# Performance work log

Measured on AMD Instinct MI355X. Metric: run time of the kernel, lower is better.

Reference implementation:

```python
import jax, jax.numpy as jnp
import numpy as np

B, H, V, MSG_MAX_LEN = 16384, 512, 32, 20


def setup_inputs() -> dict:
    key = jax.random.key(0)
    ks = jax.random.split(key, 8)
    s = 0.05  # weight scale so softmax stays well-conditioned
    return {
        "encoder_hidden": jax.random.normal(ks[0], (B, H), jnp.float32),
        "encoder_cell": jax.random.normal(ks[1], (B, H), jnp.float32),
        "W_ih": jax.random.normal(ks[2], (4 * H, V), jnp.float32) * s,
        "b_ih": jax.random.normal(ks[3], (4 * H,), jnp.float32) * s,
        "W_hh": jax.random.normal(ks[4], (4 * H, H), jnp.float32) * s,
        "b_hh": jax.random.normal(ks[5], (4 * H,), jnp.float32) * s,
        "W_out": jax.random.normal(ks[6], (V, H), jnp.float32) * s,
        "b_out": jax.random.normal(ks[7], (V,), jnp.float32) * s,
        "init_input": jnp.zeros((1, V), jnp.float32),
        "eos_idx": 31,
    }


def reference(encoder_hidden, encoder_cell, W_ih, b_ih, W_hh, b_hh, W_out, b_out, init_input, eos_idx):
    batch = encoder_hidden.shape[0]
    vocab = W_out.shape[0]
    # Original code never updates decoder_input (typo 'deocder_input'), so the
    # LSTM input is init_input every step -> input projection is loop-invariant.
    x = jnp.broadcast_to(init_input, (batch, init_input.shape[1]))
    x_proj = x @ W_ih.T + b_ih  # [B, 4H]

    def step(carry, _):
        h, c, mask, lp = carry  # h,c: [B,H]; mask: [1,B]; lp: scalar
        mask_out = mask  # mask is appended BEFORE the update in the original
        gates = x_proj + h @ W_hh.T + b_hh
        i, f, g, o = jnp.split(gates, 4, axis=1)  # torch LSTMCell gate order i,f,g,o
        i = jax.nn.sigmoid(i); f = jax.nn.sigmoid(f)
        g = jnp.tanh(g); o = jax.nn.sigmoid(o)
        c = f * c + i * g
        h = o * jnp.tanh(c)
        probs = jax.nn.softmax(h @ W_out.T + b_out, axis=1)  # [B,V]
        predict = jax.nn.one_hot(jnp.argmax(probs, axis=1), vocab, dtype=probs.dtype)  # eval-mode branch
        lp = lp + jnp.log((probs * predict).sum(axis=1)) @ mask[0]
        new_mask = mask * (1.0 - predict[:, eos_idx])  # zero out finished sequences
        return (h, c, new_mask, lp), (predict, mask_out)

    init = (encoder_hidden, encoder_cell,
            jnp.ones((1, batch), encoder_hidden.dtype),
            jnp.zeros((), encoder_hidden.dtype))
    (_, _, _, log_probs), (message, mask) = jax.lax.scan(step, init, None, length=MSG_MAX_LEN)
    return message, mask, log_probs  # [L,B,V], [L,1,B], scalar
```

## Files before the change

kernel.cpp:

```cpp
#include <hip/hip_runtime.h>
#include <math.h>

#define BATCH 16384
#define HDIM  512
#define VOCAB 32
#define STEPS 20
#define G4    2048

typedef _Float16 f16;
typedef _Float16 f16x8 __attribute__((ext_vector_type(8)));
typedef float    f32x16 __attribute__((ext_vector_type(16)));

#define SH   256.0f
#define SW   1024.0f
#define SINV (1.0f / (SH * SW))


__device__ __forceinline__ void gload16(const void* g, void* l) {
#if defined(__has_builtin) && __has_builtin(__builtin_amdgcn_global_load_lds)
    __builtin_amdgcn_global_load_lds(
        (const __attribute__((address_space(1))) void*)g,
        (__attribute__((address_space(3))) void*)l, 16, 0, 0);
#else
    *(float4*)l = *(const float4*)g;
#endif
}

__device__ __forceinline__ float fsig(float x)  { return 1.0f / (1.0f + __expf(-x)); }
__device__ __forceinline__ float ftanh(float x) { return 1.0f - 2.0f / (__expf(2.0f * x) + 1.0f); }

__global__ void init_xb_kernel(const float* __restrict__ W_ih,
                               const float* __restrict__ b_ih,
                               const float* __restrict__ b_hh,
                               const float* __restrict__ x0,
                               float* __restrict__ xb) {
    int n = blockIdx.x * blockDim.x + threadIdx.x;
    if (n >= G4) return;
    float s = b_ih[n] + b_hh[n];
    const float* wr = W_ih + (size_t)n * VOCAB;
    #pragma unroll
    for (int v = 0; v < VOCAB; v++) s += wr[v] * x0[v];
    xb[n] = s;
}

__global__ void init_mask_kernel(float* __restrict__ mask) {
    int b = blockIdx.x * blockDim.x + threadIdx.x;
    if (b < BATCH) mask[b] = 1.0f;
}

__global__ void wimg_kernel(const float* __restrict__ W_hh,
                            f16* __restrict__ Wh, f16* __restrict__ Wl) {
    size_t g  = (size_t)blockIdx.x * 256 + threadIdx.x;
    int ln = g & 63;  size_t r = g >> 6;
    int gg = r & 3;   size_t r2 = r >> 2;
    int ks = r2 & 1;  size_t r3 = r2 >> 1;
    int kc = r3 & 15; int jb = (int)(r3 >> 4);
    int n = gg * 512 + jb * 32 + (ln & 31);
    int k = kc * 32 + ks * 16 + (ln >> 5) * 8;
    const float* s = W_hh + (size_t)n * HDIM + k;
    f16x8 vh, vl;
    #pragma unroll
    for (int i = 0; i < 8; i++) {
        float x = s[i] * SW;
        f16 h = (f16)x;
        vh[i] = h;
        vl[i] = (f16)(x - (float)h);
    }
    *(f16x8*)(Wh + g * 8) = vh;
    *(f16x8*)(Wl + g * 8) = vl;
}

__global__ void woutimg_kernel(const float* __restrict__ W_out,
                               f16* __restrict__ Oh, f16* __restrict__ Ol) {
    int g  = blockIdx.x * 256 + threadIdx.x;
    int ln = g & 63;
    int r  = g >> 6;
    int kc = r >> 1, ks = r & 1;
    int v  = ln & 31;
    int k  = kc * 32 + ks * 16 + (ln >> 5) * 8;
    const float* s = W_out + (size_t)v * HDIM + k;
    f16x8 vh, vl;
    #pragma unroll
    for (int i = 0; i < 8; i++) {
        float x = s[i] * SW;
        f16 h = (f16)x;
        vh[i] = h;
        vl[i] = (f16)(x - (float)h);
    }
    *(f16x8*)(Oh + (size_t)g * 8) = vh;
    *(f16x8*)(Ol + (size_t)g * 8) = vl;
}

__global__ void hT_init_kernel(const float* __restrict__ src,
                               f16* __restrict__ dh, f16* __restrict__ dl) {
    size_t g = (size_t)blockIdx.x * 256 + threadIdx.x;
    int ln = g & 63;  size_t r = g >> 6;
    int mb = (int)(r & 511); int kk = (int)(r >> 9);
    int m = mb * 32 + (ln & 31);
    int k = kk * 16 + (ln >> 5) * 8;
    const float* s = src + (size_t)m * HDIM + k;
    f16x8 vh, vl;
    #pragma unroll
    for (int i = 0; i < 8; i++) {
        float x = s[i] * SH;
        f16 h = (f16)x;
        vh[i] = h;
        vl[i] = (f16)(x - (float)h);
    }
    *(f16x8*)(dh + g * 8) = vh;
    *(f16x8*)(dl + g * 8) = vl;
}

__device__ __forceinline__ void out_body(int lane, int mb,
        const f16* __restrict__ hTh, const f16* __restrict__ hTl,
        const f16* __restrict__ Oh,  const f16* __restrict__ Ol,
        const float* __restrict__ b_out,
        float* __restrict__ mask, float* __restrict__ msg_t,
        float* __restrict__ maskout_t, float* __restrict__ lp_part, int eos) {
    const int half = lane >> 5;
    const int l31  = lane & 31;

    f32x16 acc;
    #pragma unroll
    for (int r = 0; r < 16; r++) acc[r] = 0.0f;

    f16x8 ah[3][2], al[3][2], bh[3][2], bl[3][2];
    auto load_frags = [&](int kc, int buf) {
        #pragma unroll
        for (int ks = 0; ks < 2; ks++) {
            size_t ga = ((size_t)(kc * 2 + ks) * 512 + mb) * 64 + lane;
            size_t gb = ((size_t)(kc * 2 + ks)) * 64 + lane;
            ah[buf][ks] = *(const f16x8*)(hTh + ga * 8);
            al[buf][ks] = *(const f16x8*)(hTl + ga * 8);
            bh[buf][ks] = *(const f16x8*)(Oh + gb * 8);
            bl[buf][ks] = *(const f16x8*)(Ol + gb * 8);
        }
    };

    load_frags(0, 0);
    load_frags(1, 1);
    for (int kc = 0; kc < 16; kc++) {
        if (kc < 14) load_frags(kc + 2, (kc + 2) % 3);
        int b = kc % 3;
        #pragma unroll
        for (int ks = 0; ks < 2; ks++) {
            acc = __builtin_amdgcn_mfma_f32_32x32x16_f16(ah[b][ks], bh[b][ks], acc, 0, 0, 0);
            acc = __builtin_amdgcn_mfma_f32_32x32x16_f16(ah[b][ks], bl[b][ks], acc, 0, 0, 0);
            acc = __builtin_amdgcn_mfma_f32_32x32x16_f16(al[b][ks], bh[b][ks], acc, 0, 0, 0);
        }
    }

    const float bo = b_out[l31];
    const int   m0 = mb * 32;
    float lpacc = 0.0f;

    #pragma unroll
    for (int reg = 0; reg < 16; reg++) {
        int row = (reg & 3) + 8 * (reg >> 2) + 4 * half;
        int m   = m0 + row;
        float logit = acc[reg] * SINV + bo;

        float mval = logit;
        int   midx = l31;
        #pragma unroll
        for (int off = 16; off > 0; off >>= 1) {
            float ov = __shfl_xor(mval, off, 32);
            int   oi = __shfl_xor(midx, off, 32);
            if (ov > mval || (ov == mval && oi < midx)) { mval = ov; midx = oi; }
        }
        float s = __expf(logit - mval);
        #pragma unroll
        for (int off = 16; off > 0; off >>= 1) s += __shfl_xor(s, off, 32);

        msg_t[(size_t)m * VOCAB + l31] = (l31 == midx) ? 1.0f : 0.0f;
        if (l31 == 0) {
            float mo = mask[m];
            maskout_t[m] = mo;
            lpacc += mo * (-__logf(s));
            if (midx == eos) mask[m] = 0.0f;
        }
    }
    lpacc += __shfl_xor(lpacc, 32);
    if (lane == 0) lp_part[mb] = lpacc;
}

__global__ __launch_bounds__(256, 4)
void step_fused(const f16* __restrict__ hT_h, const f16* __restrict__ hT_l,
                f16* __restrict__ hTo_h, f16* __restrict__ hTo_l,
                const float* __restrict__ c_in,
                float* __restrict__ c_out,
                const f16* __restrict__ Wimg_h, const f16* __restrict__ Wimg_l,
                const float* __restrict__ xb,
                const f16* __restrict__ Oh, const f16* __restrict__ Ol,
                const float* __restrict__ b_out,
                float* __restrict__ mask,
                float* __restrict__ msg_p,
                float* __restrict__ maskout_p,
                float* __restrict__ lp_p,
                const int* __restrict__ eos_ptr,
                int has_out) {
    __shared__ __align__(16) char smem_raw[32768];
    f16* Blds = (f16*)smem_raw;

    const int tid  = threadIdx.x;
    const int lane = tid & 63;
    const int wave = tid >> 6;
    const int bid  = blockIdx.x;

    if (bid < 128) {
        if (!has_out) return;
        int mb = bid * 4 + wave;
        out_body(lane, mb, hT_h, hT_l, Oh, Ol, b_out,
                 mask, msg_p, maskout_p, lp_p, *eos_ptr);
        return;
    }

    const int gb   = bid - 128;
    const int jb   = gb & 15;
    const int mt   = gb >> 4;
    const int spw  = wave >> 1;
    const int ksw  = wave & 1;
    const int mbA  = mt * 4 + wave;
    const int m0   = mt * 128;
    const int j0   = jb * 32;
    const int half = lane >> 5;
    const int l31  = lane & 31;

    f32x16 acc[4];
    #pragma unroll
    for (int g = 0; g < 4; g++)
        #pragma unroll
        for (int r = 0; r < 16; r++) acc[g][r] = 0.0f;

    const f16* bsrc0 = (spw ? Wimg_l : Wimg_h)
                     + ((size_t)jb * 128 + ksw * 4) * 512 + lane * 8;
    f16* bdst0 = Blds + (size_t)(spw * 8 + ksw * 4) * 512 + lane * 8;

    auto stage_b = [&](int kc, int buf) {
        const f16* s = bsrc0 + (size_t)kc * 4096;
        f16* d = bdst0 + buf * 16 * 512;
        #pragma unroll
        for (int g = 0; g < 4; g++)
            gload16(s + g * 512, d + g * 512);
    };

    const size_t abase0 = (size_t)mbA * 512 + lane * 8;
    auto load_ah = [&](int kc, f16x8 (&dst)[2]) {
        #pragma unroll
        for (int ks = 0; ks < 2; ks++)
            dst[ks] = *(const f16x8*)(hT_h + abase0
                           + (size_t)(kc * 2 + ks) * (512 * 512));
    };
    auto load_al = [&](int kc, f16x8 (&dst)[2]) {
        #pragma unroll
        for (int ks = 0; ks < 2; ks++)
            dst[ks] = *(const f16x8*)(hT_l + abase0
                           + (size_t)(kc * 2 + ks) * (512 * 512));
    };

    auto compute = [&](f16x8 (&ah)[2], f16x8 (&al)[2], int buf) {
        #pragma unroll
        for (int ks = 0; ks < 2; ks++) {
            f16x8 bh[4], bl[4];
            #pragma unroll
            for (int g = 0; g < 4; g++) {
                bh[g] = *(const f16x8*)(Blds + (size_t)(buf * 16 + ks * 4 + g) * 512 + lane * 8);
                bl[g] = *(const f16x8*)(Blds + (size_t)(buf * 16 + 8 + ks * 4 + g) * 512 + lane * 8);
            }
            #pragma unroll
            for (int g = 0; g < 4; g++)
                acc[g] = __builtin_amdgcn_mfma_f32_32x32x16_f16(ah[ks], bh[g], acc[g], 0, 0, 0);
            #pragma unroll
            for (int g = 0; g < 4; g++)
                acc[g] = __builtin_amdgcn_mfma_f32_32x32x16_f16(ah[ks], bl[g], acc[g], 0, 0, 0);
            #pragma unroll
            for (int g = 0; g < 4; g++)
                acc[g] = __builtin_amdgcn_mfma_f32_32x32x16_f16(al[ks], bh[g], acc[g], 0, 0, 0);
        }
    };

    f16x8 ah0[2], ah1[2], al0[2], al1[2];
    stage_b(0, 0);
    load_ah(0, ah0);
    load_al(0, al0);
    for (int kc2 = 0; kc2 < 8; kc2++) {
        const int kc = kc2 * 2;
        __syncthreads();
        stage_b(kc + 1, 1);
        load_ah(kc + 1, ah1);
        load_al(kc + 1, al1);
        compute(ah0, al0, 0);
        __syncthreads();
        stage_b(kc + 2, 0);
        load_ah(kc + 2, ah0);
        load_al(kc + 2, al0);
        compute(ah1, al1, 1);
    }

    __syncthreads();
    unsigned int* hstage = (unsigned int*)smem_raw;

    const float xbi = xb[0 * HDIM + j0 + l31];
    const float xbf = xb[1 * HDIM + j0 + l31];
    const float xbg = xb[2 * HDIM + j0 + l31];
    const float xbo = xb[3 * HDIM + j0 + l31];
    #pragma unroll
    for (int reg = 0; reg < 16; reg++) {
        int row = (reg & 3) + 8 * (reg >> 2) + 4 * half;
        int ml  = wave * 32 + row;
        float gi = acc[0][reg] * SINV + xbi;
        float gf = acc[1][reg] * SINV + xbf;
        float gg = acc[2][reg] * SINV + xbg;
        float go = acc[3][reg] * SINV + xbo;
        float si = fsig(gi);
        float sf = fsig(gf);
        float tg = ftanh(gg);
        float so = fsig(go);
        size_t idx = (size_t)(m0 + ml) * HDIM + j0 + l31;
        float cn = sf * c_in[idx] + si * tg;
        c_out[idx] = cn;
        float hs = so * ftanh(cn) * SH;
        f16 hh = (f16)hs;
        f16 hl = (f16)(hs - (float)hh);
        union { f16 h[2]; unsigned int u; } pk;
        pk.h[0] = hh; pk.h[1] = hl;
        hstage[ml * 33 + l31] = pk.u;
    }
    __syncthreads();

    #pragma unroll
    for (int s = 0; s < 2; s++) {
        int q   = tid + s * 256;
        int ksp = q >> 8;
        int mbl = (q >> 6) & 3;
        int ln  = q & 63;
        int mrow = mbl * 32 + (ln & 31);
        int jj8  = ksp * 16 + (ln >> 5) * 8;
        f16x8 vh, vl;
        #pragma unroll
        for (int i = 0; i < 8; i++) {
            union { unsigned int u; f16 h[2]; } pk;
            pk.u = hstage[mrow * 33 + jj8 + i];
            vh[i] = pk.h[0];
            vl[i] = pk.h[1];
        }
        size_t gq = ((size_t)(jb * 2 + ksp) * 512 + mt * 4 + mbl) * 64 + ln;
        *(f16x8*)(hTo_h + gq * 8) = vh;
        *(f16x8*)(hTo_l + gq * 8) = vl;
    }
}

__global__ __launch_bounds__(64)
void out_mfma(const f16* __restrict__ hTh, const f16* __restrict__ hTl,
              const f16* __restrict__ Oh, const f16* __restrict__ Ol,
              const float* __restrict__ b_out,
              float* __restrict__ mask,
              float* __restrict__ msg_t,
              float* __restrict__ maskout_t,
              float* __restrict__ lp_part,
              const int* __restrict__ eos_ptr) {
    out_body(threadIdx.x, blockIdx.x, hTh, hTl, Oh, Ol, b_out,
             mask, msg_t, maskout_t, lp_part, *eos_ptr);
}

__global__ void reduce_lp_kernel(const float* __restrict__ parts, int n,
                                 float* __restrict__ out) {
    __shared__ float sm[256];
    float s = 0.0f;
    for (int i = threadIdx.x; i < n; i += 256) s += parts[i];
    sm[threadIdx.x] = s;
    __syncthreads();
    for (int off = 128; off > 0; off >>= 1) {
        if (threadIdx.x < off) sm[threadIdx.x] += sm[threadIdx.x + off];
        __syncthreads();
    }
    if (threadIdx.x == 0) *out = sm[0];
}

extern "C" void kernel_launch(void* const* d_in, const int* in_sizes, int n_in,
                              void* d_out, int out_size, void* d_ws, size_t ws_size,
                              hipStream_t stream) {
    const float* enc_h  = (const float*)d_in[0];
    const float* enc_c  = (const float*)d_in[1];
    const float* W_ih   = (const float*)d_in[2];
    const float* b_ih   = (const float*)d_in[3];
    const float* W_hh   = (const float*)d_in[4];
    const float* b_hh   = (const float*)d_in[5];
    const float* W_out  = (const float*)d_in[6];
    const float* b_out  = (const float*)d_in[7];
    const float* x0     = (const float*)d_in[8];
    const int*   eosP   = (const int*)d_in[9];

    float* out     = (float*)d_out;
    float* msg     = out;
    float* maskout = out + (size_t)STEPS * BATCH * VOCAB;
    float* lp_out  = maskout + (size_t)STEPS * BATCH;

    const size_t NH = (size_t)BATCH * HDIM;
    char* w = (char*)d_ws;
    f16* hTh_a = (f16*)w;            w += NH * sizeof(f16);
    f16* hTl_a = (f16*)w;            w += NH * sizeof(f16);
    f16* hTh_b = (f16*)w;            w += NH * sizeof(f16);
    f16* hTl_b = (f16*)w;            w += NH * sizeof(f16);
    float* cbuf = (float*)w;         w += NH * sizeof(float);
    f16* Wimg_h = (f16*)w;           w += (size_t)G4 * HDIM * sizeof(f16);
    f16* Wimg_l = (f16*)w;           w += (size_t)G4 * HDIM * sizeof(f16);
    f16* Wout_h = (f16*)w;           w += (size_t)VOCAB * HDIM * sizeof(f16);
    f16* Wout_l = (f16*)w;           w += (size_t)VOCAB * HDIM * sizeof(f16);
    float* xb = (float*)w;           w += G4 * sizeof(float);
    float* maskbuf = (float*)w;      w += BATCH * sizeof(float);
    float* lp_parts = (float*)w;

    init_mask_kernel<<<(BATCH + 255) / 256, 256, 0, stream>>>(maskbuf);
    init_xb_kernel<<<(G4 + 255) / 256, 256, 0, stream>>>(W_ih, b_ih, b_hh, x0, xb);
    wimg_kernel<<<(G4 * HDIM / 8) / 256, 256, 0, stream>>>(W_hh, Wimg_h, Wimg_l);
    woutimg_kernel<<<8, 256, 0, stream>>>(W_out, Wout_h, Wout_l);
    hT_init_kernel<<<(int)((NH / 8) / 256), 256, 0, stream>>>(enc_h, hTh_a, hTl_a);

    for (int t = 0; t < STEPS; t++) {
        const f16* hi_in = (t & 1) ? hTh_b : hTh_a;
        const f16* lo_in = (t & 1) ? hTl_b : hTl_a;
        f16* hi_out      = (t & 1) ? hTh_a : hTh_b;
        f16* lo_out      = (t & 1) ? hTl_a : hTl_b;
        const float* cin = (t == 0) ? enc_c : cbuf;
        int tp = (t > 0) ? (t - 1) : 0;
        step_fused<<<2176, 256, 0, stream>>>(
            hi_in, lo_in, hi_out, lo_out, cin, cbuf, Wimg_h, Wimg_l, xb,
            Wout_h, Wout_l, b_out, maskbuf,
            msg + (size_t)tp * BATCH * VOCAB,
            maskout + (size_t)tp * BATCH,
            lp_parts + (size_t)tp * 512,
            eosP, t > 0 ? 1 : 0);
    }
    {
        const f16* hi = (STEPS & 1) ? hTh_b : hTh_a;
        const f16* lo = (STEPS & 1) ? hTl_b : hTl_a;
        out_mfma<<<512, 64, 0, stream>>>(
            hi, lo, Wout_h, Wout_l, b_out, maskbuf,
            msg + (size_t)(STEPS - 1) * BATCH * VOCAB,
            maskout + (size_t)(STEPS - 1) * BATCH,
            lp_parts + (size_t)(STEPS - 1) * 512,
            eosP);
    }
    reduce_lp_kernel<<<1, 256, 0, stream>>>(lp_parts, STEPS * 512, lp_out);
}
```

Measured before the change: 2.430 ms.

## Load W_hh fragments directly from global into registers, dropping LDS staging

The recurrent GEMM no longer stages the weight tiles through shared memory with async global-to-LDS copies and barriers. Each wave now loads its A and B fragments straight from global memory into a two-deep register ring and runs the split-precision MFMAs without any __syncthreads. This removes the barriers and the LDS round trip. The cost is more registers (occupancy bound lowered from 4 to 3) and four waves each reading the same weight fragments through cache instead of once per block.

New measurement: 2.901 ms. 19.4% more time.

```diff
diff --git a/kernel.cpp b/kernel.cpp
--- a/kernel.cpp
+++ b/kernel.cpp
@@ -15,16 +15,6 @@
 #define SW   1024.0f
 #define SINV (1.0f / (SH * SW))
 
-
-__device__ __forceinline__ void gload16(const void* g, void* l) {
-#if defined(__has_builtin) && __has_builtin(__builtin_amdgcn_global_load_lds)
-    __builtin_amdgcn_global_load_lds(
-        (const __attribute__((address_space(1))) void*)g,
-        (__attribute__((address_space(3))) void*)l, 16, 0, 0);
-#else
-    *(float4*)l = *(const float4*)g;
-#endif
-}
 
 __device__ __forceinline__ float fsig(float x)  { return 1.0f / (1.0f + __expf(-x)); }
 __device__ __forceinline__ float ftanh(float x) { return 1.0f - 2.0f / (__expf(2.0f * x) + 1.0f); }
@@ -184,7 +174,7 @@
     if (lane == 0) lp_part[mb] = lpacc;
 }
 
-__global__ __launch_bounds__(256, 4)
+__global__ __launch_bounds__(256, 3)
 void step_fused(const f16* __restrict__ hT_h, const f16* __restrict__ hT_l,
                 f16* __restrict__ hTo_h, f16* __restrict__ hTo_l,
                 const float* __restrict__ c_in,
@@ -199,8 +189,7 @@
                 float* __restrict__ lp_p,
                 const int* __restrict__ eos_ptr,
                 int has_out) {
-    __shared__ __align__(16) char smem_raw[32768];
-    f16* Blds = (f16*)smem_raw;
+    __shared__ __align__(16) char smem_raw[16896];
 
     const int tid  = threadIdx.x;
     const int lane = tid & 63;
@@ -218,8 +207,6 @@
     const int gb   = bid - 128;
     const int jb   = gb & 15;
     const int mt   = gb >> 4;
-    const int spw  = wave >> 1;
-    const int ksw  = wave & 1;
     const int mbA  = mt * 4 + wave;
     const int m0   = mt * 128;
     const int j0   = jb * 32;
@@ -232,72 +219,41 @@
         #pragma unroll
         for (int r = 0; r < 16; r++) acc[g][r] = 0.0f;
 
-    const f16* bsrc0 = (spw ? Wimg_l : Wimg_h)
-                     + ((size_t)jb * 128 + ksw * 4) * 512 + lane * 8;
-    f16* bdst0 = Blds + (size_t)(spw * 8 + ksw * 4) * 512 + lane * 8;
-
-    auto stage_b = [&](int kc, int buf) {
-        const f16* s = bsrc0 + (size_t)kc * 4096;
-        f16* d = bdst0 + buf * 16 * 512;
+    const f16* aHp = hT_h + (size_t)mbA * 512 + lane * 8;
+    const f16* aLp = hT_l + (size_t)mbA * 512 + lane * 8;
+    const f16* bHp = Wimg_h + (size_t)jb * 128 * 512 + lane * 8;
+    const f16* bLp = Wimg_l + (size_t)jb * 128 * 512 + lane * 8;
+    const size_t ASTRIDE = (size_t)512 * 512;
+    const size_t BSTRIDE = (size_t)4 * 512;
+
+    f16x8 ah[2], al[2], bh[2][4], bl[2][4];
+    auto load_u = [&](int u, int s) {
+        ah[s] = *(const f16x8*)(aHp + (size_t)u * ASTRIDE);
+        al[s] = *(const f16x8*)(aLp + (size_t)u * ASTRIDE);
+        #pragma unroll
+        for (int g = 0; g < 4; g++) {
+            bh[s][g] = *(const f16x8*)(bHp + (size_t)u * BSTRIDE + g * 512);
+            bl[s][g] = *(const f16x8*)(bLp + (size_t)u * BSTRIDE + g * 512);
+        }
+    };
+
+    load_u(0, 0);
+    load_u(1, 1);
+    #pragma unroll 2
+    for (int u = 0; u < 32; u++) {
+        const int s = u & 1;
         #pragma unroll
         for (int g = 0; g < 4; g++)
-            gload16(s + g * 512, d + g * 512);
-    };
-
-    const size_t abase0 = (size_t)mbA * 512 + lane * 8;
-    auto load_ah = [&](int kc, f16x8 (&dst)[2]) {
-        #pragma unroll
-        for (int ks = 0; ks < 2; ks++)
-            dst[ks] = *(const f16x8*)(hT_h + abase0
-                           + (size_t)(kc * 2 + ks) * (512 * 512));
-    };
-    auto load_al = [&](int kc, f16x8 (&dst)[2]) {
-        #pragma unroll
-        for (int ks = 0; ks < 2; ks++)
-            dst[ks] = *(const f16x8*)(hT_l + abase0
-                           + (size_t)(kc * 2 + ks) * (512 * 512));
-    };
-
-    auto compute = [&](f16x8 (&ah)[2], f16x8 (&al)[2], int buf) {
-        #pragma unroll
-        for (int ks = 0; ks < 2; ks++) {
-            f16x8 bh[4], bl[4];
-            #pragma unroll
-            for (int g = 0; g < 4; g++) {
-                bh[g] = *(const f16x8*)(Blds + (size_t)(buf * 16 + ks * 4 + g) * 512 + lane * 8);
-                bl[g] = *(const f16x8*)(Blds + (size_t)(buf * 16 + 8 + ks * 4 + g) * 512 + lane * 8);
-            }
-            #pragma unroll
-            for (int g = 0; g < 4; g++)
-                acc[g] = __builtin_amdgcn_mfma_f32_32x32x16_f16(ah[ks], bh[g], acc[g], 0, 0, 0);
-            #pragma unroll
-            for (int g = 0; g < 4; g++)
-                acc[g] = __builtin_amdgcn_mfma_f32_32x32x16_f16(ah[ks], bl[g], acc[g], 0, 0, 0);
-            #pragma unroll
-            for (int g = 0; g < 4; g++)
-                acc[g] = __builtin_amdgcn_mfma_f32_32x32x16_f16(al[ks], bh[g], acc[g], 0, 0, 0);
-        }
-    };
-
-    f16x8 ah0[2], ah1[2], al0[2], al1[2];
-    stage_b(0, 0);
-    load_ah(0, ah0);
-    load_al(0, al0);
-    for (int kc2 = 0; kc2 < 8; kc2++) {
-        const int kc = kc2 * 2;
-        __syncthreads();
-        stage_b(kc + 1, 1);
-        load_ah(kc + 1, ah1);
-        load_al(kc + 1, al1);
-        compute(ah0, al0, 0);
-        __syncthreads();
-        stage_b(kc + 2, 0);
-        load_ah(kc + 2, ah0);
-        load_al(kc + 2, al0);
-        compute(ah1, al1, 1);
-    }
-
-    __syncthreads();
+            acc[g] = __builtin_amdgcn_mfma_f32_32x32x16_f16(ah[s], bh[s][g], acc[g], 0, 0, 0);
+        #pragma unroll
+        for (int g = 0; g < 4; g++)
+            acc[g] = __builtin_amdgcn_mfma_f32_32x32x16_f16(ah[s], bl[s][g], acc[g], 0, 0, 0);
+        #pragma unroll
+        for (int g = 0; g < 4; g++)
+            acc[g] = __builtin_amdgcn_mfma_f32_32x32x16_f16(al[s], bh[s][g], acc[g], 0, 0, 0);
+        if (u < 30) load_u(u + 2, s);
+    }
+
     unsigned int* hstage = (unsigned int*)smem_raw;
 
     const float xbi = xb[0 * HDIM + j0 + l31];
```
